# Optimization experiments

Measured on AMD Instinct MI355X. Metric: run time of the kernel, lower is better.

Reference implementation:

```python
import jax, jax.numpy as jnp
import numpy as np

B, N, P = 8, 4096, 1024
P4 = P // 4
EPS = 1e-5


def _ln(x, g, b):
    mu = jnp.mean(x, axis=-1, keepdims=True)
    var = jnp.var(x, axis=-1, keepdims=True)
    return (x - mu) * jax.lax.rsqrt(var + EPS) * g + b


def setup_inputs() -> dict:
    key = jax.random.key(0)
    ks = jax.random.split(key, 16)
    s = lambda fan: 1.0 / np.sqrt(fan)
    return {
        "xyz": jax.random.normal(ks[0], (B, N, 3), jnp.float32),
        "x": jax.random.normal(ks[1], (B, N, P), jnp.float32),
        "ln1_g": jnp.ones((P,), jnp.float32),
        "ln1_b": jnp.zeros((P,), jnp.float32),
        "ln2_g": jnp.ones((P,), jnp.float32),
        "ln2_b": jnp.zeros((P,), jnp.float32),
        "qk_w": jax.random.normal(ks[2], (P4, P), jnp.float32) * s(P),   # shared q/k 1x1 conv, no bias
        "v_w": jax.random.normal(ks[3], (P, P), jnp.float32) * s(P),
        "v_b": jax.random.normal(ks[4], (P,), jnp.float32) * s(P),
        "t1_w": jax.random.normal(ks[5], (P, P4), jnp.float32) * s(P4),  # trans_conv
        "t1_b": jax.random.normal(ks[6], (P,), jnp.float32) * s(P4),
        "t2_w": jax.random.normal(ks[7], (P, P4), jnp.float32) * s(P4),  # trans_conv1
        "t2_b": jax.random.normal(ks[8], (P,), jnp.float32) * s(P4),
        "m1_w": jax.random.normal(ks[9], (P, P), jnp.float32) * s(P),
        "m1_b": jax.random.normal(ks[10], (P,), jnp.float32) * s(P),
        "m2_w": jax.random.normal(ks[11], (P, P), jnp.float32) * s(P),
        "m2_b": jax.random.normal(ks[12], (P,), jnp.float32) * s(P),
    }


def reference(xyz, x, ln1_g, ln1_b, ln2_g, ln2_b, qk_w, v_w, v_b,
              t1_w, t1_b, t2_w, t2_b, m1_w, m1_b, m2_w, m2_b):
    # xyz is accepted but unused, matching the torch module. Dropout = eval identity.
    res1 = x
    h = _ln(x, ln1_g, ln1_b)                                   # [B,N,P]
    # TransformerBlock_1 (1x1 convs on h^T [B,P,N] are just matmuls over P)
    x_q = jnp.einsum('op,bnp->bon', qk_w, h)                   # [B,P4,N]
    # k shares weights with q; x_k permuted is x_q transposed
    x_v = jnp.einsum('op,bnp->bno', v_w, h) + v_b              # [B,N,P]
    energy = jnp.einsum('bqn,bkn->bqk', x_q, x_q)              # [B,P4,P4]
    att = jnp.einsum('op,bpk->bok', t1_w, energy) + t1_b[:, None]   # [B,P,P4]
    att = jax.nn.gelu(att, approximate=False)
    att = jnp.einsum('op,bkp->bok', t2_w, att) + t2_b[:, None]      # [B,P,P]
    att = jax.nn.softmax(att, axis=-1)
    t_out = jnp.einsum('bnp,bpq->bnq', x_v, att)               # [B,N,P]
    x1 = t_out + res1
    h2 = _ln(x1, ln2_g, ln2_b)
    m = jax.nn.gelu(h2 @ m1_w.T + m1_b, approximate=False)
    m = m @ m2_w.T + m2_b
    return x1 + m
```

## Files before the change

### kernel.cpp

```cpp
#include <hip/hip_runtime.h>


typedef __attribute__((ext_vector_type(4))) float f32x4;
typedef __attribute__((ext_vector_type(4))) unsigned int u32x4;
typedef __attribute__((ext_vector_type(8))) _Float16 h16x8;
typedef __attribute__((ext_vector_type(8))) unsigned short u16x8;
typedef __attribute__((ext_vector_type(4))) unsigned short u16x4;

__device__ __forceinline__ unsigned short f2h(float f) {
  _Float16 h = (_Float16)f;
  return __builtin_bit_cast(unsigned short, h);
}
__device__ __forceinline__ float h2f(unsigned short u) {
  return (float)__builtin_bit_cast(_Float16, u);
}
__device__ __forceinline__ unsigned split16(float f) {
  _Float16 h = (_Float16)f;
  _Float16 l = (_Float16)(f - (float)h);
  return (unsigned)__builtin_bit_cast(unsigned short, h) |
         ((unsigned)__builtin_bit_cast(unsigned short, l) << 16);
}
__device__ __forceinline__ float gelu_f(float x) {
  return 0.5f * x * (1.0f + erff(x * 0.70710678118654752f));
}
__device__ __forceinline__ void gload16(const void* g, void* l) {
  __builtin_amdgcn_global_load_lds(
      (const __attribute__((address_space(1))) unsigned int*)g,
      (__attribute__((address_space(3))) unsigned int*)l, 16, 0, 0);
}
#define FENCE() asm volatile("" ::: "memory")

__device__ __forceinline__ void xcd_swz(int& bx, int& by, int gx, int gy) {
  const int nwg = gx * gy;
  if ((nwg & 7) == 0 && nwg >= 16) {
    const int flat = bx + gx * by;
    const int chunk = nwg >> 3;
    const int nf = (flat & 7) * chunk + (flat >> 3);
    bx = nf % gx;
    by = nf / gx;
  }
}

__global__ __launch_bounds__(256)
void ln_kernel(const float* __restrict__ x, const float* __restrict__ g,
               const float* __restrict__ b, unsigned short* __restrict__ hi,
               unsigned short* __restrict__ lo) {
  __shared__ float red[16];
  const size_t base = (size_t)blockIdx.x * 1024;
  const int t = threadIdx.x;
  f32x4 v = *(const f32x4*)&x[base + t * 4];
  float s = v[0] + v[1] + v[2] + v[3];
  float q = v[0] * v[0] + v[1] * v[1] + v[2] * v[2] + v[3] * v[3];
#pragma unroll
  for (int o = 32; o > 0; o >>= 1) { s += __shfl_down(s, o); q += __shfl_down(q, o); }
  const int w = t >> 6;
  if ((t & 63) == 0) { red[w] = s; red[8 + w] = q; }
  __syncthreads();
  s = (red[0] + red[1]) + (red[2] + red[3]);
  q = (red[8] + red[9]) + (red[10] + red[11]);
  const float mu = s * (1.0f / 1024.0f);
  const float var = q * (1.0f / 1024.0f) - mu * mu;
  const float is = rsqrtf(var + 1e-5f);
  f32x4 gg = *(const f32x4*)&g[t * 4];
  f32x4 bb = *(const f32x4*)&b[t * 4];
  u16x4 oh, ol;
#pragma unroll
  for (int j = 0; j < 4; j++) {
    float y = (v[j] - mu) * is * gg[j] + bb[j];
    unsigned p = split16(y);
    oh[j] = (unsigned short)(p & 0xffffu);
    ol[j] = (unsigned short)(p >> 16);
  }
  *(u16x4*)&hi[base + t * 4] = oh;
  if (lo) *(u16x4*)&lo[base + t * 4] = ol;
}

__global__ __launch_bounds__(256)
void ln16_kernel(const unsigned short* __restrict__ x16, const float* __restrict__ g,
                 const float* __restrict__ b, unsigned short* __restrict__ hi) {
  __shared__ float red[16];
  const size_t base = (size_t)blockIdx.x * 1024;
  const int t = threadIdx.x;
  u16x4 raw = *(const u16x4*)&x16[base + t * 4];
  float v[4];
#pragma unroll
  for (int j = 0; j < 4; j++) v[j] = h2f(raw[j]);
  float s = v[0] + v[1] + v[2] + v[3];
  float q = v[0] * v[0] + v[1] * v[1] + v[2] * v[2] + v[3] * v[3];
#pragma unroll
  for (int o = 32; o > 0; o >>= 1) { s += __shfl_down(s, o); q += __shfl_down(q, o); }
  const int w = t >> 6;
  if ((t & 63) == 0) { red[w] = s; red[8 + w] = q; }
  __syncthreads();
  s = (red[0] + red[1]) + (red[2] + red[3]);
  q = (red[8] + red[9]) + (red[10] + red[11]);
  const float mu = s * (1.0f / 1024.0f);
  const float var = q * (1.0f / 1024.0f) - mu * mu;
  const float is = rsqrtf(var + 1e-5f);
  f32x4 gg = *(const f32x4*)&g[t * 4];
  f32x4 bb = *(const f32x4*)&b[t * 4];
  u16x4 oh;
#pragma unroll
  for (int j = 0; j < 4; j++) oh[j] = f2h((v[j] - mu) * is * gg[j] + bb[j]);
  *(u16x4*)&hi[base + t * 4] = oh;
}

__global__ __launch_bounds__(256)
void cvt_kernel(const float* __restrict__ in, unsigned short* __restrict__ hi,
                unsigned short* __restrict__ lo, int n4) {
  int i = blockIdx.x * 256 + threadIdx.x;
  if (i < n4) {
    f32x4 v = *(const f32x4*)&in[(size_t)i * 4];
    u16x4 oh, ol;
#pragma unroll
    for (int j = 0; j < 4; j++) {
      unsigned p = split16(v[j]);
      oh[j] = (unsigned short)(p & 0xffffu);
      ol[j] = (unsigned short)(p >> 16);
    }
    *(u16x4*)&hi[(size_t)i * 4] = oh;
    if (lo) *(u16x4*)&lo[(size_t)i * 4] = ol;
  }
}

template <int EPI>
__global__ __launch_bounds__(256)
void gemm_v(const unsigned short* __restrict__ Ain, const unsigned short* __restrict__ Bin,
            void* __restrict__ Cout, const float* __restrict__ bias,
            const unsigned short* __restrict__ res16In,
            int K, int lda, int ldb, int ldc,
            long long sA, long long sB, long long sC, long long sRes) {
  __shared__ short As[2][4096];
  __shared__ short Bs[2][4096];
  const int z = blockIdx.z;
  const unsigned short* A = Ain + (size_t)z * sA;
  const unsigned short* B = Bin + (size_t)z * sB;
  int bx = blockIdx.x, by = blockIdx.y;
  xcd_swz(bx, by, gridDim.x, gridDim.y);
  const int mBase = by * 128, nBase = bx * 128;
  const int t = threadIdx.x, w = t >> 6, l = t & 63;
  const int r16 = l & 15, kq = l >> 4;
  const int wr = (w >> 1) * 64, wc = (w & 1) * 64;
  f32x4 acc[4][4] = {};

  auto stage = [&](int buf, int k0) {
#pragma unroll
    for (int i = 0; i < 2; ++i) {
      const int c = i * 256 + t;
      const int row = c >> 2, cc = c & 3;
      const int gc = cc ^ ((row >> 1) & 3);
      short* la = &As[buf][(i * 256 + w * 64) * 8];
      short* lb = &Bs[buf][(i * 256 + w * 64) * 8];
      gload16(&A[(size_t)(mBase + row) * lda + k0 + gc * 8], la);
      gload16(&B[(size_t)(nBase + row) * ldb + k0 + gc * 8], lb);
    }
  };

  const int nt = K >> 5;
  stage(0, 0);
  if (nt > 1) stage(1, 32);
  for (int ts = 0; ts < nt; ++ts) {
    const int cur = ts & 1;
    if (ts + 1 < nt) { asm volatile("s_waitcnt vmcnt(4)" ::: "memory"); }
    else             { asm volatile("s_waitcnt vmcnt(0)" ::: "memory"); }
    __builtin_amdgcn_s_barrier();
    FENCE();
    h16x8 aF[4], bF[4];
#pragma unroll
    for (int mi = 0; mi < 4; mi++) {
      const int r = wr + mi * 16 + r16;
      aF[mi] = *(const h16x8*)&As[cur][r * 32 + (kq ^ ((r >> 1) & 3)) * 8];
    }
#pragma unroll
    for (int ni = 0; ni < 4; ni++) {
      const int r = wc + ni * 16 + r16;
      bF[ni] = *(const h16x8*)&Bs[cur][r * 32 + (kq ^ ((r >> 1) & 3)) * 8];
    }
    __builtin_amdgcn_s_setprio(1);
#pragma unroll
    for (int mi = 0; mi < 4; mi++)
#pragma unroll
      for (int ni = 0; ni < 4; ni++)
        acc[mi][ni] = __builtin_amdgcn_mfma_f32_16x16x32_f16(aF[mi], bF[ni], acc[mi][ni], 0, 0, 0);
    __builtin_amdgcn_s_setprio(0);
    FENCE();
    __builtin_amdgcn_s_barrier();
    FENCE();
    if (ts + 2 < nt) stage(cur, (ts + 2) * 32);
  }

  unsigned short* C16 = (unsigned short*)Cout + (size_t)z * sC;
  float* C32 = (float*)Cout + (size_t)z * sC;
  const unsigned short* res16 = (EPI == 3) ? (res16In + (size_t)z * sRes) : nullptr;
#pragma unroll
  for (int mi = 0; mi < 4; mi++) {
#pragma unroll
    for (int ni = 0; ni < 4; ni++) {
      const int cl = nBase + wc + ni * 16 + r16;
      const float bcol = bias[cl];
#pragma unroll
      for (int r = 0; r < 4; r++) {
        const int rw = mBase + wr + mi * 16 + kq * 4 + r;
        float v = acc[mi][ni][r] + bcol;
        if (EPI == 1) v = gelu_f(v);
        const size_t idx = (size_t)rw * ldc + cl;
        if (EPI == 3) { v += h2f(res16[idx]); C32[idx] = v; }
        else          C16[idx] = f2h(v);
      }
    }
  }
}

__global__ __launch_bounds__(256)
void gemm_r(const unsigned short* __restrict__ Ain, const unsigned short* __restrict__ Bin,
            unsigned short* __restrict__ Cout, const float* __restrict__ resIn,
            int K, int lda, int ldb, int ldc,
            long long sA, long long sB, long long sC, long long sRes) {
  __shared__ short As[2][4096];
  __shared__ short Bs[2][4096];
  const int z = blockIdx.z;
  const unsigned short* A = Ain + (size_t)z * sA;
  const unsigned short* B = Bin + (size_t)z * sB;
  int bx = blockIdx.x, by = blockIdx.y;
  xcd_swz(bx, by, gridDim.x, gridDim.y);
  const int mBase = by * 128, nBase = bx * 128;
  const int t = threadIdx.x, w = t >> 6, l = t & 63;
  const int r16 = l & 15, kq = l >> 4;
  const int wr = (w >> 1) * 64, wc = (w & 1) * 64;
  f32x4 acc[4][4] = {};

  u32x4 ra0, ra1, rb0, rb1;
  auto loadreg = [&](int k0) {
#pragma unroll
    for (int i = 0; i < 2; ++i) {
      const int c = i * 256 + t;
      const int row = c >> 2, cc = c & 3;
      const int gc = cc ^ ((row >> 1) & 3);
      u32x4 va = *(const u32x4*)&A[(size_t)(mBase + row) * lda + k0 + gc * 8];
      u32x4 vb = *(const u32x4*)&B[(size_t)(nBase + row) * ldb + k0 + gc * 8];
      if (i == 0) { ra0 = va; rb0 = vb; } else { ra1 = va; rb1 = vb; }
    }
  };
  auto dswrite = [&](int buf) {
    *(u32x4*)&As[buf][t * 8] = ra0;
    *(u32x4*)&Bs[buf][t * 8] = rb0;
    *(u32x4*)&As[buf][(256 + t) * 8] = ra1;
    *(u32x4*)&Bs[buf][(256 + t) * 8] = rb1;
  };

  const int nt = K >> 5;
  loadreg(0);
  dswrite(0);
  if (nt > 1) loadreg(32);
  asm volatile("s_waitcnt lgkmcnt(0)" ::: "memory");
  __builtin_amdgcn_s_barrier();
  FENCE();
  for (int ts = 0; ts < nt; ++ts) {
    const int cur = ts & 1;
    h16x8 aF[4], bF[4];
#pragma unroll
    for (int mi = 0; mi < 4; mi++) {
      const int r = wr + mi * 16 + r16;
      aF[mi] = *(const h16x8*)&As[cur][r * 32 + (kq ^ ((r >> 1) & 3)) * 8];
    }
#pragma unroll
    for (int ni = 0; ni < 4; ni++) {
      const int r = wc + ni * 16 + r16;
      bF[ni] = *(const h16x8*)&Bs[cur][r * 32 + (kq ^ ((r >> 1) & 3)) * 8];
    }
    __builtin_amdgcn_s_setprio(1);
#pragma unroll
    for (int mi = 0; mi < 4; mi++)
#pragma unroll
      for (int ni = 0; ni < 4; ni++)
        acc[mi][ni] = __builtin_amdgcn_mfma_f32_16x16x32_f16(aF[mi], bF[ni], acc[mi][ni], 0, 0, 0);
    __builtin_amdgcn_s_setprio(0);
    FENCE();
    if (ts + 1 < nt) {
      __builtin_amdgcn_s_barrier();
      FENCE();
      dswrite((ts + 1) & 1);
      if (ts + 2 < nt) loadreg((ts + 2) * 32);
      asm volatile("s_waitcnt lgkmcnt(0)" ::: "memory");
      FENCE();
      __builtin_amdgcn_s_barrier();
      FENCE();
    }
  }

  unsigned short* C16 = Cout + (size_t)z * sC;
  const float* res = resIn + (size_t)z * sRes;
#pragma unroll
  for (int mi = 0; mi < 4; mi++) {
#pragma unroll
    for (int ni = 0; ni < 4; ni++) {
      const int cl = nBase + wc + ni * 16 + r16;
#pragma unroll
      for (int r = 0; r < 4; r++) {
        const int rw = mBase + wr + mi * 16 + kq * 4 + r;
        const size_t idx = (size_t)rw * ldc + cl;
        C16[idx] = f2h(acc[mi][ni][r] + res[idx]);
      }
    }
  }
}

template <int EPI>
__global__ __launch_bounds__(256)
void gemm_s(const unsigned short* __restrict__ Ahi, const unsigned short* __restrict__ Alo,
            const unsigned short* __restrict__ Bhi, const unsigned short* __restrict__ Blo,
            void* __restrict__ Cout, unsigned short* __restrict__ Cout2,
            const float* __restrict__ bias,
            int K, int lda, int ldb, int ldc,
            long long sA, long long sB, long long sC, int splitK) {
  __shared__ short As[2][8192];
  __shared__ short Bs[2][8192];
  const int z = blockIdx.z;
  const int bi = z / splitK, sp = z % splitK;
  const int kLen = K / splitK, kStart = sp * kLen;
  const unsigned short* AH = Ahi + (size_t)bi * sA;
  const unsigned short* BH = Bhi + (size_t)bi * sB;
  const unsigned short* AL = Alo + (size_t)bi * sA;
  const unsigned short* BL = Blo + (size_t)bi * sB;
  int bx = blockIdx.x, by = blockIdx.y;
  xcd_swz(bx, by, gridDim.x, gridDim.y);
  const int mBase = by * 128, nBase = bx * 128;
  const int t = threadIdx.x, w = t >> 6, l = t & 63;
  const int r16 = l & 15, kq = l >> 4;
  const int wr = (w >> 1) * 64, wc = (w & 1) * 64;
  f32x4 acc[4][4] = {};

  auto stage = [&](int buf, int k0) {
#pragma unroll
    for (int i = 0; i < 2; ++i) {
      const int c = i * 256 + t;
      const int row = c >> 2, cc = c & 3;
      const int gc = cc ^ ((row >> 1) & 3);
      const int cbase = i * 256 + w * 64;
      const size_t ga = (size_t)(mBase + row) * lda + k0 + gc * 8;
      const size_t gb = (size_t)(nBase + row) * ldb + k0 + gc * 8;
      gload16(&AH[ga], &As[buf][cbase * 8]);
      gload16(&AL[ga], &As[buf][4096 + cbase * 8]);
      gload16(&BH[gb], &Bs[buf][cbase * 8]);
      gload16(&BL[gb], &Bs[buf][4096 + cbase * 8]);
    }
  };

  const int nsteps = kLen >> 5;
  stage(0, kStart);
  if (nsteps > 1) stage(1, kStart + 32);
  for (int ts = 0; ts < nsteps; ++ts) {
    const int cur = ts & 1;
    if (ts + 1 < nsteps) { asm volatile("s_waitcnt vmcnt(8)" ::: "memory"); }
    else                 { asm volatile("s_waitcnt vmcnt(0)" ::: "memory"); }
    __builtin_amdgcn_s_barrier();
    FENCE();
    h16x8 aH[4], bH[4], aL[4], bL[4];
#pragma unroll
    for (int mi = 0; mi < 4; mi++) {
      const int r = wr + mi * 16 + r16;
      const int off = r * 32 + (kq ^ ((r >> 1) & 3)) * 8;
      aH[mi] = *(const h16x8*)&As[cur][off];
      aL[mi] = *(const h16x8*)&As[cur][4096 + off];
    }
#pragma unroll
    for (int ni = 0; ni < 4; ni++) {
      const int r = wc + ni * 16 + r16;
      const int off = r * 32 + (kq ^ ((r >> 1) & 3)) * 8;
      bH[ni] = *(const h16x8*)&Bs[cur][off];
      bL[ni] = *(const h16x8*)&Bs[cur][4096 + off];
    }
    __builtin_amdgcn_s_setprio(1);
#pragma unroll
    for (int mi = 0; mi < 4; mi++)
#pragma unroll
      for (int ni = 0; ni < 4; ni++) {
        acc[mi][ni] = __builtin_amdgcn_mfma_f32_16x16x32_f16(aH[mi], bH[ni], acc[mi][ni], 0, 0, 0);
        acc[mi][ni] = __builtin_amdgcn_mfma_f32_16x16x32_f16(aH[mi], bL[ni], acc[mi][ni], 0, 0, 0);
        acc[mi][ni] = __builtin_amdgcn_mfma_f32_16x16x32_f16(aL[mi], bH[ni], acc[mi][ni], 0, 0, 0);
      }
    __builtin_amdgcn_s_setprio(0);
    FENCE();
    __builtin_amdgcn_s_barrier();
    FENCE();
    if (ts + 2 < nsteps) stage(cur, kStart + (ts + 2) * 32);
  }

  unsigned short* C16 = (unsigned short*)Cout + (size_t)z * sC;
  unsigned short* C16b = Cout2 ? Cout2 + (size_t)z * sC : nullptr;
  float* C32 = (float*)Cout + (size_t)z * sC;
#pragma unroll
  for (int mi = 0; mi < 4; mi++) {
#pragma unroll
    for (int ni = 0; ni < 4; ni++) {
      const int cl = nBase + wc + ni * 16 + r16;
#pragma unroll
      for (int r = 0; r < 4; r++) {
        const int rw = mBase + wr + mi * 16 + kq * 4 + r;
        float v = acc[mi][ni][r];
        if (EPI == 6 || EPI == 7) v += bias[rw];
        if (EPI == 6) v = gelu_f(v);
        const size_t idx = (size_t)rw * ldc + cl;
        if (EPI == 4 || EPI == 6) {
          unsigned p = split16(v);
          C16[idx] = (unsigned short)(p & 0xffffu);
          C16b[idx] = (unsigned short)(p >> 16);
        } else {
          C32[idx] = v;
        }
      }
    }
  }
}

__global__ __launch_bounds__(256)
void ereduce_kernel(const float* __restrict__ part, unsigned short* __restrict__ ehi,
                    unsigned short* __restrict__ elo) {
  const size_t idx = (size_t)blockIdx.x * 256 + threadIdx.x;
  const size_t b = idx >> 16, i = idx & 65535;
  const float* p = part + b * (8ull * 65536) + i;
  float s0 = (p[0] + p[65536]) + (p[2 * 65536] + p[3 * 65536]);
  float s1 = (p[4 * 65536] + p[5 * 65536]) + (p[6 * 65536] + p[7 * 65536]);
  unsigned pk = split16(s0 + s1);
  ehi[idx] = (unsigned short)(pk & 0xffffu);
  elo[idx] = (unsigned short)(pk >> 16);
}

__global__ __launch_bounds__(256)
void smax_t_kernel(const float* __restrict__ a2, unsigned short* __restrict__ attT) {
  __shared__ float S[8][1028];
  __shared__ float inv[8];
  const int t = threadIdx.x;
  const int b = blockIdx.y;
  const int o0 = blockIdx.x * 8;
  const float* src = a2 + ((size_t)b * 1024 + o0) * 1024;
#pragma unroll
  for (int i = 0; i < 8; i++)
    *(f32x4*)&S[i][t * 4] = *(const f32x4*)&src[(size_t)i * 1024 + t * 4];
  __syncthreads();
  const int w = t >> 6, l = t & 63;
  for (int rr = 0; rr < 2; rr++) {
    const int r = w * 2 + rr;
    float m = -1e30f;
#pragma unroll
    for (int i = 0; i < 16; i++) m = fmaxf(m, S[r][l + i * 64]);
#pragma unroll
    for (int o = 32; o > 0; o >>= 1) m = fmaxf(m, __shfl_xor(m, o));
    float ssum = 0.0f;
#pragma unroll
    for (int i = 0; i < 16; i++) {
      float e = expf(S[r][l + i * 64] - m);
      S[r][l + i * 64] = e;
      ssum += e;
    }
#pragma unroll
    for (int o = 32; o > 0; o >>= 1) ssum += __shfl_xor(ssum, o);
    if (l == 0) inv[r] = 1.0f / ssum;
  }
  __syncthreads();
  float iv[8];
#pragma unroll
  for (int r = 0; r < 8; r++) iv[r] = inv[r];
#pragma unroll
  for (int i = 0; i < 4; i++) {
    const int k = i * 256 + t;
    u16x8 ov;
#pragma unroll
    for (int r = 0; r < 8; r++) ov[r] = f2h(S[r][k] * iv[r]);
    *(u16x8*)&attT[((size_t)b * 1024 + k) * 1024 + o0] = ov;
  }
}

extern "C" void kernel_launch(void* const* d_in, const int* in_sizes, int n_in,
                              void* d_out, int out_size, void* d_ws, size_t ws_size,
                              hipStream_t stream) {
  (void)in_sizes; (void)n_in; (void)out_size; (void)ws_size;
  const float* x     = (const float*)d_in[1];
  const float* ln1_g = (const float*)d_in[2];
  const float* ln1_b = (const float*)d_in[3];
  const float* ln2_g = (const float*)d_in[4];
  const float* ln2_b = (const float*)d_in[5];
  const float* qk_w  = (const float*)d_in[6];
  const float* v_w   = (const float*)d_in[7];
  const float* v_b   = (const float*)d_in[8];
  const float* t1_w  = (const float*)d_in[9];
  const float* t1_b  = (const float*)d_in[10];
  const float* t2_w  = (const float*)d_in[11];
  const float* t2_b  = (const float*)d_in[12];
  const float* m1_w  = (const float*)d_in[13];
  const float* m1_b  = (const float*)d_in[14];
  const float* m2_w  = (const float*)d_in[15];
  const float* m2_b  = (const float*)d_in[16];

  char* ws = (char*)d_ws;
  unsigned short* hhi  = (unsigned short*)(ws + 0);
  unsigned short* hlo  = (unsigned short*)(ws + 67108864);
  unsigned short* Qthi = (unsigned short*)(ws + 134217728);
  unsigned short* Qtlo = (unsigned short*)(ws + 150994944);
  float*          part = (float*)(ws + 167772160);
  unsigned short* Ehi  = (unsigned short*)(ws + 184549376);
  unsigned short* Elo  = (unsigned short*)(ws + 185597952);
  unsigned short* Ghi  = (unsigned short*)(ws + 186646528);
  unsigned short* Glo  = (unsigned short*)(ws + 190840832);
  float*          a2   = (float*)(ws + 195035136);
  unsigned short* attT = (unsigned short*)(ws + 228589568);
  unsigned short* xv   = (unsigned short*)(ws + 245366784);
  unsigned short* x1h  = (unsigned short*)(ws + 312475648);
  unsigned short* wqh  = (unsigned short*)(ws + 446693376);
  unsigned short* wql  = (unsigned short*)(ws + 447217664);
  unsigned short* wv   = (unsigned short*)(ws + 447741952);
  unsigned short* wt1h = (unsigned short*)(ws + 449839104);
  unsigned short* wt1l = (unsigned short*)(ws + 450363392);
  unsigned short* wt2h = (unsigned short*)(ws + 450887680);
  unsigned short* wt2l = (unsigned short*)(ws + 451411968);
  unsigned short* wm1  = (unsigned short*)(ws + 451936256);
  unsigned short* wm2  = (unsigned short*)(ws + 454033408);
  unsigned short* h2 = hhi;
  unsigned short* gb = hlo;
  float* out = (float*)d_out;

  cvt_kernel<<<dim3(256),  dim3(256), 0, stream>>>(qk_w, wqh, wql, 65536);
  cvt_kernel<<<dim3(1024), dim3(256), 0, stream>>>(v_w, wv, nullptr, 262144);
  cvt_kernel<<<dim3(256),  dim3(256), 0, stream>>>(t1_w, wt1h, wt1l, 65536);
  cvt_kernel<<<dim3(256),  dim3(256), 0, stream>>>(t2_w, wt2h, wt2l, 65536);
  cvt_kernel<<<dim3(1024), dim3(256), 0, stream>>>(m1_w, wm1, nullptr, 262144);
  cvt_kernel<<<dim3(1024), dim3(256), 0, stream>>>(m2_w, wm2, nullptr, 262144);
  ln_kernel<<<dim3(32768), dim3(256), 0, stream>>>(x, ln1_g, ln1_b, hhi, hlo);
  gemm_s<4><<<dim3(32, 2, 8), dim3(256), 0, stream>>>(
      wqh, wql, hhi, hlo, Qthi, Qtlo, nullptr,
      1024, 1024, 1024, 4096, 0, 4194304, 1048576, 1);
  gemm_v<0><<<dim3(8, 256, 1), dim3(256), 0, stream>>>(
      hhi, wv, xv, v_b, nullptr, 1024, 1024, 1024, 1024, 0, 0, 0, 0);
  gemm_s<5><<<dim3(2, 2, 64), dim3(256), 0, stream>>>(
      Qthi, Qtlo, Qthi, Qtlo, part, nullptr, nullptr,
      4096, 4096, 4096, 256, 1048576, 1048576, 65536, 8);
  ereduce_kernel<<<dim3(2048), dim3(256), 0, stream>>>(part, Ehi, Elo);
  gemm_s<6><<<dim3(2, 8, 8), dim3(256), 0, stream>>>(
      wt1h, wt1l, Ehi, Elo, Ghi, Glo, t1_b,
      256, 256, 256, 256, 0, 65536, 262144, 1);
  gemm_s<7><<<dim3(8, 8, 8), dim3(256), 0, stream>>>(
      wt2h, wt2l, Ghi, Glo, a2, nullptr, t2_b,
      256, 256, 256, 1024, 0, 262144, 1048576, 1);
  smax_t_kernel<<<dim3(128, 8), dim3(256), 0, stream>>>(a2, attT);
  gemm_r<<<dim3(8, 32, 8), dim3(256), 0, stream>>>(
      xv, attT, x1h, x, 1024, 1024, 1024, 1024, 4194304, 1048576, 4194304, 4194304);
  ln16_kernel<<<dim3(32768), dim3(256), 0, stream>>>(x1h, ln2_g, ln2_b, h2);
  gemm_v<1><<<dim3(8, 256, 1), dim3(256), 0, stream>>>(
      h2, wm1, gb, m1_b, nullptr, 1024, 1024, 1024, 1024, 0, 0, 0, 0);
  gemm_v<3><<<dim3(8, 256, 1), dim3(256), 0, stream>>>(
      gb, wm2, out, m2_b, x1h, 1024, 1024, 1024, 1024, 0, 0, 0, 0);
}
```

Measured before the change: 714.1 us.

## Reassociate value projection with attention to fold V weight into per-batch matrix

Instead of computing x_v = h·Wv^T + b over all N tokens and then x_v·att, the code first forms a per-batch effective weight (att^T·Wv, 1024x1024 per batch) plus an effective bias (att^T·v_b), then applies it directly to h in one GEMM with the residual fused. This removes one full N×P×P GEMM over all tokens and the x_v intermediate, replacing it with a smaller batched P×P×P GEMM. The residual is now read from an fp16 copy of x written by the LN kernel, which trades a little accuracy for less traffic, and the XCD swizzle mapping is changed to column-major order.

```diff
diff --git a/kernel.cpp b/kernel.cpp
--- a/kernel.cpp
+++ b/kernel.cpp
@@ -2,7 +2,6 @@
 
 
 typedef __attribute__((ext_vector_type(4))) float f32x4;
-typedef __attribute__((ext_vector_type(4))) unsigned int u32x4;
 typedef __attribute__((ext_vector_type(8))) _Float16 h16x8;
 typedef __attribute__((ext_vector_type(8))) unsigned short u16x8;
 typedef __attribute__((ext_vector_type(4))) unsigned short u16x4;
@@ -33,18 +32,18 @@
 __device__ __forceinline__ void xcd_swz(int& bx, int& by, int gx, int gy) {
   const int nwg = gx * gy;
   if ((nwg & 7) == 0 && nwg >= 16) {
-    const int flat = bx + gx * by;
+    const int hw = bx + gx * by;
     const int chunk = nwg >> 3;
-    const int nf = (flat & 7) * chunk + (flat >> 3);
-    bx = nf % gx;
-    by = nf / gx;
+    const int tf = (hw & 7) * chunk + (hw >> 3);
+    by = tf % gy;
+    bx = tf / gy;
   }
 }
 
 __global__ __launch_bounds__(256)
 void ln_kernel(const float* __restrict__ x, const float* __restrict__ g,
                const float* __restrict__ b, unsigned short* __restrict__ hi,
-               unsigned short* __restrict__ lo) {
+               unsigned short* __restrict__ lo, unsigned short* __restrict__ xh) {
   __shared__ float red[16];
   const size_t base = (size_t)blockIdx.x * 1024;
   const int t = threadIdx.x;
@@ -63,16 +62,18 @@
   const float is = rsqrtf(var + 1e-5f);
   f32x4 gg = *(const f32x4*)&g[t * 4];
   f32x4 bb = *(const f32x4*)&b[t * 4];
-  u16x4 oh, ol;
+  u16x4 oh, ol, ox;
 #pragma unroll
   for (int j = 0; j < 4; j++) {
     float y = (v[j] - mu) * is * gg[j] + bb[j];
     unsigned p = split16(y);
     oh[j] = (unsigned short)(p & 0xffffu);
     ol[j] = (unsigned short)(p >> 16);
+    ox[j] = f2h(v[j]);
   }
   *(u16x4*)&hi[base + t * 4] = oh;
   if (lo) *(u16x4*)&lo[base + t * 4] = ol;
+  if (xh) *(u16x4*)&xh[base + t * 4] = ox;
 }
 
 __global__ __launch_bounds__(256)
@@ -123,13 +124,55 @@
   }
 }
 
+__global__ __launch_bounds__(256)
+void vwt_kernel(const float* __restrict__ vw, unsigned short* __restrict__ wvt) {
+  __shared__ float T[64][65];
+  const int bx = blockIdx.x, by = blockIdx.y;
+  const int t = threadIdx.x;
+  const int lr = t >> 6, lc = t & 63;
+#pragma unroll
+  for (int i = 0; i < 16; ++i) {
+    const int row = i * 4 + lr;
+    T[row][lc] = vw[(size_t)(by * 64 + row) * 1024 + bx * 64 + lc];
+  }
+  __syncthreads();
+#pragma unroll
+  for (int i = 0; i < 16; ++i) {
+    const int row = i * 4 + lr;
+    wvt[(size_t)(bx * 64 + row) * 1024 + by * 64 + lc] = f2h(T[lc][row]);
+  }
+}
+
+__global__ __launch_bounds__(256)
+void beff_kernel(const unsigned short* __restrict__ attT, const float* __restrict__ vb,
+                 float* __restrict__ beff) {
+  const int b = blockIdx.y;
+  const int q = blockIdx.x * 4 + (threadIdx.x >> 6);
+  const int l = threadIdx.x & 63;
+  const unsigned short* row = attT + ((size_t)b * 1024 + q) * 1024;
+  float s = 0.0f;
+#pragma unroll
+  for (int i = 0; i < 2; ++i) {
+    u16x8 v = *(const u16x8*)&row[(i * 64 + l) * 8];
+    f32x4 vb0 = *(const f32x4*)&vb[(i * 64 + l) * 8];
+    f32x4 vb1 = *(const f32x4*)&vb[(i * 64 + l) * 8 + 4];
+#pragma unroll
+    for (int j = 0; j < 4; j++) s += h2f(v[j]) * vb0[j];
+#pragma unroll
+    for (int j = 0; j < 4; j++) s += h2f(v[j + 4]) * vb1[j];
+  }
+#pragma unroll
+  for (int o = 32; o > 0; o >>= 1) s += __shfl_down(s, o);
+  if (l == 0) beff[b * 1024 + q] = s;
+}
+
 template <int EPI>
 __global__ __launch_bounds__(256)
 void gemm_v(const unsigned short* __restrict__ Ain, const unsigned short* __restrict__ Bin,
             void* __restrict__ Cout, const float* __restrict__ bias,
             const unsigned short* __restrict__ res16In,
             int K, int lda, int ldb, int ldc,
-            long long sA, long long sB, long long sC, long long sRes) {
+            long long sA, long long sB, long long sC, long long sBias, long long sRes) {
   __shared__ short As[2][4096];
   __shared__ short Bs[2][4096];
   const int z = blockIdx.z;
@@ -191,115 +234,23 @@
 
   unsigned short* C16 = (unsigned short*)Cout + (size_t)z * sC;
   float* C32 = (float*)Cout + (size_t)z * sC;
-  const unsigned short* res16 = (EPI == 3) ? (res16In + (size_t)z * sRes) : nullptr;
+  const float* bp = (EPI == 1 || EPI == 3 || EPI == 8) ? bias + (size_t)z * sBias : nullptr;
+  const unsigned short* rp = (EPI == 3 || EPI == 8) ? res16In + (size_t)z * sRes : nullptr;
 #pragma unroll
   for (int mi = 0; mi < 4; mi++) {
 #pragma unroll
     for (int ni = 0; ni < 4; ni++) {
       const int cl = nBase + wc + ni * 16 + r16;
-      const float bcol = bias[cl];
+      const float bcol = bp ? bp[cl] : 0.0f;
 #pragma unroll
       for (int r = 0; r < 4; r++) {
         const int rw = mBase + wr + mi * 16 + kq * 4 + r;
         float v = acc[mi][ni][r] + bcol;
         if (EPI == 1) v = gelu_f(v);
         const size_t idx = (size_t)rw * ldc + cl;
-        if (EPI == 3) { v += h2f(res16[idx]); C32[idx] = v; }
-        else          C16[idx] = f2h(v);
-      }
-    }
-  }
-}
-
-__global__ __launch_bounds__(256)
-void gemm_r(const unsigned short* __restrict__ Ain, const unsigned short* __restrict__ Bin,
-            unsigned short* __restrict__ Cout, const float* __restrict__ resIn,
-            int K, int lda, int ldb, int ldc,
-            long long sA, long long sB, long long sC, long long sRes) {
-  __shared__ short As[2][4096];
-  __shared__ short Bs[2][4096];
-  const int z = blockIdx.z;
-  const unsigned short* A = Ain + (size_t)z * sA;
-  const unsigned short* B = Bin + (size_t)z * sB;
-  int bx = blockIdx.x, by = blockIdx.y;
-  xcd_swz(bx, by, gridDim.x, gridDim.y);
-  const int mBase = by * 128, nBase = bx * 128;
-  const int t = threadIdx.x, w = t >> 6, l = t & 63;
-  const int r16 = l & 15, kq = l >> 4;
-  const int wr = (w >> 1) * 64, wc = (w & 1) * 64;
-  f32x4 acc[4][4] = {};
-
-  u32x4 ra0, ra1, rb0, rb1;
-  auto loadreg = [&](int k0) {
-#pragma unroll
-    for (int i = 0; i < 2; ++i) {
-      const int c = i * 256 + t;
-      const int row = c >> 2, cc = c & 3;
-      const int gc = cc ^ ((row >> 1) & 3);
-      u32x4 va = *(const u32x4*)&A[(size_t)(mBase + row) * lda + k0 + gc * 8];
-      u32x4 vb = *(const u32x4*)&B[(size_t)(nBase + row) * ldb + k0 + gc * 8];
-      if (i == 0) { ra0 = va; rb0 = vb; } else { ra1 = va; rb1 = vb; }
-    }
-  };
-  auto dswrite = [&](int buf) {
-    *(u32x4*)&As[buf][t * 8] = ra0;
-    *(u32x4*)&Bs[buf][t * 8] = rb0;
-    *(u32x4*)&As[buf][(256 + t) * 8] = ra1;
-    *(u32x4*)&Bs[buf][(256 + t) * 8] = rb1;
-  };
-
-  const int nt = K >> 5;
-  loadreg(0);
-  dswrite(0);
-  if (nt > 1) loadreg(32);
-  asm volatile("s_waitcnt lgkmcnt(0)" ::: "memory");
-  __builtin_amdgcn_s_barrier();
-  FENCE();
-  for (int ts = 0; ts < nt; ++ts) {
-    const int cur = ts & 1;
-    h16x8 aF[4], bF[4];
-#pragma unroll
-    for (int mi = 0; mi < 4; mi++) {
-      const int r = wr + mi * 16 + r16;
-      aF[mi] = *(const h16x8*)&As[cur][r * 32 + (kq ^ ((r >> 1) & 3)) * 8];
-    }
-#pragma unroll
-    for (int ni = 0; ni < 4; ni++) {
-      const int r = wc + ni * 16 + r16;
-      bF[ni] = *(const h16x8*)&Bs[cur][r * 32 + (kq ^ ((r >> 1) & 3)) * 8];
-    }
-    __builtin_amdgcn_s_setprio(1);
-#pragma unroll
-    for (int mi = 0; mi < 4; mi++)
-#pragma unroll
-      for (int ni = 0; ni < 4; ni++)
-        acc[mi][ni] = __builtin_amdgcn_mfma_f32_16x16x32_f16(aF[mi], bF[ni], acc[mi][ni], 0, 0, 0);
-    __builtin_amdgcn_s_setprio(0);
-    FENCE();
-    if (ts + 1 < nt) {
-      __builtin_amdgcn_s_barrier();
-      FENCE();
-      dswrite((ts + 1) & 1);
-      if (ts + 2 < nt) loadreg((ts + 2) * 32);
-      asm volatile("s_waitcnt lgkmcnt(0)" ::: "memory");
-      FENCE();
-      __builtin_amdgcn_s_barrier();
-      FENCE();
-    }
-  }
-
-  unsigned short* C16 = Cout + (size_t)z * sC;
-  const float* res = resIn + (size_t)z * sRes;
-#pragma unroll
-  for (int mi = 0; mi < 4; mi++) {
-#pragma unroll
-    for (int ni = 0; ni < 4; ni++) {
-      const int cl = nBase + wc + ni * 16 + r16;
-#pragma unroll
-      for (int r = 0; r < 4; r++) {
-        const int rw = mBase + wr + mi * 16 + kq * 4 + r;
-        const size_t idx = (size_t)rw * ldc + cl;
-        C16[idx] = f2h(acc[mi][ni][r] + res[idx]);
+        if (EPI == 3)      C32[idx] = v + h2f(rp[idx]);
+        else if (EPI == 8) C16[idx] = f2h(v + h2f(rp[idx]));
+        else               C16[idx] = f2h(v);
       }
     }
   }
@@ -504,11 +455,13 @@
   unsigned short* Glo  = (unsigned short*)(ws + 190840832);
   float*          a2   = (float*)(ws + 195035136);
   unsigned short* attT = (unsigned short*)(ws + 228589568);
-  unsigned short* xv   = (unsigned short*)(ws + 245366784);
-  unsigned short* x1h  = (unsigned short*)(ws + 312475648);
+  unsigned short* WeT  = (unsigned short*)(ws + 245366784);
+  float*          beff = (float*)(ws + 262144000);
+  unsigned short* xh   = (unsigned short*)(ws + 268435456);
+  unsigned short* x1h  = (unsigned short*)(ws + 335544320);
   unsigned short* wqh  = (unsigned short*)(ws + 446693376);
   unsigned short* wql  = (unsigned short*)(ws + 447217664);
-  unsigned short* wv   = (unsigned short*)(ws + 447741952);
+  unsigned short* wvt  = (unsigned short*)(ws + 447741952);
   unsigned short* wt1h = (unsigned short*)(ws + 449839104);
   unsigned short* wt1l = (unsigned short*)(ws + 450363392);
   unsigned short* wt2h = (unsigned short*)(ws + 450887680);
@@ -520,17 +473,15 @@
   float* out = (float*)d_out;
 
   cvt_kernel<<<dim3(256),  dim3(256), 0, stream>>>(qk_w, wqh, wql, 65536);
-  cvt_kernel<<<dim3(1024), dim3(256), 0, stream>>>(v_w, wv, nullptr, 262144);
+  vwt_kernel<<<dim3(16, 16), dim3(256), 0, stream>>>(v_w, wvt);
   cvt_kernel<<<dim3(256),  dim3(256), 0, stream>>>(t1_w, wt1h, wt1l, 65536);
   cvt_kernel<<<dim3(256),  dim3(256), 0, stream>>>(t2_w, wt2h, wt2l, 65536);
   cvt_kernel<<<dim3(1024), dim3(256), 0, stream>>>(m1_w, wm1, nullptr, 262144);
   cvt_kernel<<<dim3(1024), dim3(256), 0, stream>>>(m2_w, wm2, nullptr, 262144);
-  ln_kernel<<<dim3(32768), dim3(256), 0, stream>>>(x, ln1_g, ln1_b, hhi, hlo);
+  ln_kernel<<<dim3(32768), dim3(256), 0, stream>>>(x, ln1_g, ln1_b, hhi, hlo, xh);
   gemm_s<4><<<dim3(32, 2, 8), dim3(256), 0, stream>>>(
       wqh, wql, hhi, hlo, Qthi, Qtlo, nullptr,
       1024, 1024, 1024, 4096, 0, 4194304, 1048576, 1);
-  gemm_v<0><<<dim3(8, 256, 1), dim3(256), 0, stream>>>(
-      hhi, wv, xv, v_b, nullptr, 1024, 1024, 1024, 1024, 0, 0, 0, 0);
   gemm_s<5><<<dim3(2, 2, 64), dim3(256), 0, stream>>>(
       Qthi, Qtlo, Qthi, Qtlo, part, nullptr, nullptr,
       4096, 4096, 4096, 256, 1048576, 1048576, 65536, 8);
@@ -542,11 +493,16 @@
       wt2h, wt2l, Ghi, Glo, a2, nullptr, t2_b,
       256, 256, 256, 1024, 0, 262144, 1048576, 1);
   smax_t_kernel<<<dim3(128, 8), dim3(256), 0, stream>>>(a2, attT);
-  gemm_r<<<dim3(8, 32, 8), dim3(256), 0, stream>>>(
-      xv, attT, x1h, x, 1024, 1024, 1024, 1024, 4194304, 1048576, 4194304, 4194304);
+  gemm_v<4><<<dim3(8, 8, 8), dim3(256), 0, stream>>>(
+      attT, wvt, WeT, nullptr, nullptr,
+      1024, 1024, 1024, 1024, 1048576, 0, 1048576, 0, 0);
+  beff_kernel<<<dim3(256, 8), dim3(256), 0, stream>>>(attT, v_b, beff);
+  gemm_v<8><<<dim3(8, 32, 8), dim3(256), 0, stream>>>(
+      hhi, WeT, x1h, beff, xh,
+      1024, 1024, 1024, 1024, 4194304, 1048576, 4194304, 1024, 4194304);
   ln16_kernel<<<dim3(32768), dim3(256), 0, stream>>>(x1h, ln2_g, ln2_b, h2);
   gemm_v<1><<<dim3(8, 256, 1), dim3(256), 0, stream>>>(
-      h2, wm1, gb, m1_b, nullptr, 1024, 1024, 1024, 1024, 0, 0, 0, 0);
+      h2, wm1, gb, m1_b, nullptr, 1024, 1024, 1024, 1024, 0, 0, 0, 0, 0);
   gemm_v<3><<<dim3(8, 256, 1), dim3(256), 0, stream>>>(
-      gb, wm2, out, m2_b, x1h, 1024, 1024, 1024, 1024, 0, 0, 0, 0);
-}
+      gb, wm2, out, m2_b, x1h, 1024, 1024, 1024, 1024, 0, 0, 0, 0, 0);
+}
```

Result: faster. 684.0 us (-4.2%).
